# Performance work log

Measured on AMD Instinct MI355X. Metric: run time of the kernel, lower is better.

Reference implementation:

```python
import jax, jax.numpy as jnp
import numpy as np

BITS = 16          # number of histogram bins == number of spiking time steps
B, IN_DIM, HID = 16384, 784, 128


def setup_inputs() -> dict:
    key = jax.random.key(0)
    ks = jax.random.split(key, 9)
    dims = [(HID, IN_DIM), (HID, HID), (HID, HID), (IN_DIM, HID)]
    inp = {"features": jax.random.uniform(ks[0], (B, IN_DIM), jnp.float32)}
    for i, (o, d) in enumerate(dims):
        inp["W%d" % i] = jax.random.normal(ks[1 + i], (o, d), jnp.float32) * 0.05
        inp["b%d" % i] = jax.random.normal(ks[5 + i], (o,), jnp.float32) * 0.05
    # np.histogram_bin_edges(bins=16) -> 17 uniformly spaced edges per layer
    in_max = [1.0, 4.0, 4.0, 4.0]
    out_max = [4.0, 4.0, 4.0, 4.0]
    for i in range(4):
        inp["in_bins%d" % i] = jnp.linspace(0.0, in_max[i], BITS + 1, dtype=jnp.float32)
        inp["out_bins%d" % i] = jnp.linspace(0.0, out_max[i], BITS + 1, dtype=jnp.float32)
    return inp


def _spike(t):
    # output[output>1]=1; output[output<1]=0  (==1 stays 1)  -> (t >= 1)
    # totals[output==1] -= 1
    s = (t >= 1.0).astype(t.dtype)
    return s, t - s


def _forward(features, Ws, bs, in_bins, out_bins):
    h_in = [e[1] - e[0] for e in in_bins]    # uniform spike heights
    h_out = [e[1] - e[0] for e in out_bins]
    # set_up_weights: weight *= h_in; weight /= h_out (bias likewise)
    Weff = [Ws[l] * (h_in[l] / h_out[l]) for l in range(4)]
    beff = [bs[l] * (h_in[l] / h_out[l]) for l in range(4)]
    n = features.shape[0]
    # discretize: np.digitize(x, in_bins) - 1, then / 16.0 (non-differentiable)
    act = (jnp.digitize(jax.lax.stop_gradient(features), in_bins[0]) - 1).astype(features.dtype) / BITS
    t_in = jnp.zeros_like(features)                               # input-layer membrane
    totals = tuple(jnp.broadcast_to(beff[l], (n,) + beff[l].shape) for l in range(4))  # reset_totals: totals = bias
    out_acc = jnp.zeros((n, Weff[3].shape[0]), features.dtype)

    def step(carry, _):
        t_in, t0, t1, t2, t3, out = carry
        s_in, t_in = _spike(t_in + act)
        # process_layer: totals += sum(weight * spikes, axis=1) == spikes @ W.T
        s0, t0 = _spike(t0 + s_in @ Weff[0].T)
        s1, t1 = _spike(t1 + s0 @ Weff[1].T)
        s2, t2 = _spike(t2 + s1 @ Weff[2].T)
        s3, t3 = _spike(t3 + s2 @ Weff[3].T)
        return (t_in, t0, t1, t2, t3, out + s3), None

    carry, _ = jax.lax.scan(step, (t_in,) + totals + (out_acc,), None, length=BITS)
    out_spikes = carry[-1]
    # decoder_output_layer.reconstruct: spikes * (out_bins[1] - out_bins[0])
    return out_spikes * h_out[3]


def reference(features, W0, W1, W2, W3, b0, b1, b2, b3,
              in_bins0, in_bins1, in_bins2, in_bins3,
              out_bins0, out_bins1, out_bins2, out_bins3):
    return _forward(features,
                    [W0, W1, W2, W3], [b0, b1, b2, b3],
                    [in_bins0, in_bins1, in_bins2, in_bins3],
                    [out_bins0, out_bins1, out_bins2, out_bins3])
```

## Files before the change

### kernel.cpp

```cpp
#include <hip/hip_runtime.h>

#define IN_DIM 784
#define HID 128
#define NSTEP 16
#define BATCH 16384

typedef float v2f __attribute__((ext_vector_type(2)));
typedef float v4f __attribute__((ext_vector_type(4)));

constexpr int W0T_OFF = 0;
constexpr int W1T_OFF = W0T_OFF + IN_DIM*HID;
constexpr int W2T_OFF = W1T_OFF + HID*HID;
constexpr int W3T_OFF = W2T_OFF + HID*HID;
constexpr int B0_OFF  = W3T_OFF + HID*IN_DIM;
constexpr int B1_OFF  = B0_OFF + HID;
constexpr int B2_OFF  = B1_OFF + HID;
constexpr int B3_OFF  = B2_OFF + HID;
constexpr int WS_FLOATS = B3_OFF + IN_DIM;

constexpr int CHUNK_COLS = 32;
constexpr int CHUNK_F    = CHUNK_COLS * HID;
constexpr int NCHUNK     = 25;

constexpr int TPB   = 512;
constexpr int WAVES = TPB / 64;

__global__ __launch_bounds__(256) void prep_kernel(
    const float* __restrict__ W0, const float* __restrict__ b0,
    const float* __restrict__ W1, const float* __restrict__ b1,
    const float* __restrict__ W2, const float* __restrict__ b2,
    const float* __restrict__ W3, const float* __restrict__ b3,
    const float* __restrict__ ib0, const float* __restrict__ ob0,
    const float* __restrict__ ib1, const float* __restrict__ ob1,
    const float* __restrict__ ib2, const float* __restrict__ ob2,
    const float* __restrict__ ib3, const float* __restrict__ ob3,
    float* __restrict__ ws)
{
    int idx = blockIdx.x * 256 + threadIdx.x;
    if (idx >= WS_FLOATS) return;
    float r0 = (ib0[1] - ib0[0]) / (ob0[1] - ob0[0]);
    float r1 = (ib1[1] - ib1[0]) / (ob1[1] - ob1[0]);
    float r2 = (ib2[1] - ib2[0]) / (ob2[1] - ob2[0]);
    float r3 = (ib3[1] - ib3[0]) / (ob3[1] - ob3[0]);
    if (idx < W1T_OFF) {
        int t = idx;            int k = t >> 7, j = t & 127;
        ws[idx] = W0[j * IN_DIM + k] * r0;
    } else if (idx < W2T_OFF) {
        int t = idx - W1T_OFF;  int k = t >> 7, j = t & 127;
        ws[idx] = W1[j * HID + k] * r1;
    } else if (idx < W3T_OFF) {
        int t = idx - W2T_OFF;  int k = t >> 7, j = t & 127;
        ws[idx] = W2[j * HID + k] * r2;
    } else if (idx < B0_OFF) {
        int t = idx - W3T_OFF;  int k = t / IN_DIM, o = t % IN_DIM;
        ws[idx] = W3[o * HID + k] * r3;
    } else if (idx < B1_OFF) ws[idx] = b0[idx - B0_OFF] * r0;
    else if (idx < B2_OFF)   ws[idx] = b1[idx - B1_OFF] * r1;
    else if (idx < B3_OFF)   ws[idx] = b2[idx - B2_OFF] * r2;
    else                     ws[idx] = b3[idx - B3_OFF] * r3;
}

__global__ __launch_bounds__(TPB) void snn_main(
    const float* __restrict__ feat,
    const float* __restrict__ ws,
    const float* __restrict__ ib0,
    const float* __restrict__ ob3,
    float* __restrict__ out)
{
    __shared__ float smem[2 * CHUNK_F];

    const int tid  = threadIdx.x;
    const int lane = tid & 63;
    const int wid  = tid >> 6;
    const int sample = blockIdx.x * WAVES + wid;

    const float* W0t = ws + W0T_OFF;
    const float* W1t = ws + W1T_OFF;
    const float* W2t = ws + W2T_OFF;
    const float* W3t = ws + W3T_OFF;
    const float* frow = feat + (size_t)sample * IN_DIM;

    float edge[16];
#pragma unroll
    for (int e = 0; e < 16; ++e) edge[e] = ib0[e + 1];

    {
        const float4* g4 = (const float4*)W0t;
        float4* lb = (float4*)smem;
#pragma unroll
        for (int i = 0; i < 2; ++i) lb[i * TPB + tid] = g4[i * TPB + tid];
    }
    __syncthreads();

    v2f C[16];
#pragma unroll
    for (int mv = 0; mv < 16; ++mv) C[mv] = (v2f)(0.f);

    for (int c = 0; c < NCHUNK; ++c) {
        float4 rg0, rg1;
        {
            const float4* g4 = (const float4*)W0t + (size_t)(c + 1) * (CHUNK_F / 4);
            rg0 = g4[0 * TPB + tid];
            rg1 = g4[1 * TPB + tid];
        }

        int col = c * CHUNK_COLS + (lane & 31);
        bool valid = col < IN_DIM;
        float x = frow[valid ? col : 0];
        int mm = 0;
#pragma unroll
        for (int e = 0; e < 16; ++e) mm += (x >= edge[e]) ? 1 : 0;
        if (!valid) mm = -1;

        const v2f* bufp = (const v2f*)(smem + (c & 1) * CHUNK_F);
#pragma unroll
        for (int mv = 1; mv <= 16; ++mv) {
            unsigned mk = (unsigned)__ballot(mm == mv);
            v2f ca = (v2f)(0.f), cb = (v2f)(0.f);
            while (mk) {
                int b0 = __builtin_ctz(mk); mk &= mk - 1;
                v2f w0 = bufp[b0 * 64 + lane];
                if (mk) {
                    int b1 = __builtin_ctz(mk); mk &= mk - 1;
                    v2f w1 = bufp[b1 * 64 + lane];
                    if (mk) {
                        int b2 = __builtin_ctz(mk); mk &= mk - 1;
                        v2f w2 = bufp[b2 * 64 + lane];
                        if (mk) {
                            int b3i = __builtin_ctz(mk); mk &= mk - 1;
                            v2f w3 = bufp[b3i * 64 + lane];
                            cb += w3;
                        }
                        ca += w2;
                    }
                    cb += w1;
                }
                ca += w0;
            }
            C[mv - 1] += ca + cb;
        }

        if (c + 1 < NCHUNK) {
            float4* lb = (float4*)(smem + ((c + 1) & 1) * CHUNK_F);
            lb[0 * TPB + tid] = rg0;
            lb[1 * TPB + tid] = rg1;
        }
        __syncthreads();
    }

    v2f t0 = ((const v2f*)(ws + B0_OFF))[lane];
    v2f t1 = ((const v2f*)(ws + B1_OFF))[lane];
    v2f t2 = ((const v2f*)(ws + B2_OFF))[lane];
    v4f t3[4], cnt[4];
    {
        const v4f* b3v = (const v4f*)(ws + B3_OFF);
#pragma unroll
        for (int r = 0; r < 3; ++r) t3[r] = b3v[r * 64 + lane];
        t3[3] = (v4f)(0.f);
        if (lane < 4) t3[3] = b3v[192 + lane];
#pragma unroll
        for (int r = 0; r < 4; ++r) cnt[r] = (v4f)(0.f);
    }

    for (int s = 1; s <= NSTEP; ++s) {
#pragma unroll
        for (int mv = 1; mv <= 16; ++mv) {
            if (((s * mv) & 15) < mv) t0 += C[mv - 1];
        }
        {
            bool px = (t0.x >= 1.0f), py = (t0.y >= 1.0f);
            unsigned long long mx = __ballot(px);
            unsigned long long my = __ballot(py);
            if (px) t0.x -= 1.0f;
            if (py) t0.y -= 1.0f;
            v2f ca = (v2f)(0.f), cb = (v2f)(0.f);
            while (mx) {
                int b0 = __builtin_amdgcn_readfirstlane(__builtin_ctzll(mx)); mx &= mx - 1;
                v2f w0 = ((const v2f*)(W1t + (2 * b0) * HID))[lane];
                if (mx) {
                    int b1 = __builtin_amdgcn_readfirstlane(__builtin_ctzll(mx)); mx &= mx - 1;
                    v2f w1 = ((const v2f*)(W1t + (2 * b1) * HID))[lane];
                    if (mx) {
                        int b2 = __builtin_amdgcn_readfirstlane(__builtin_ctzll(mx)); mx &= mx - 1;
                        v2f w2 = ((const v2f*)(W1t + (2 * b2) * HID))[lane];
                        if (mx) {
                            int b3i = __builtin_amdgcn_readfirstlane(__builtin_ctzll(mx)); mx &= mx - 1;
                            v2f w3 = ((const v2f*)(W1t + (2 * b3i) * HID))[lane];
                            cb += w3;
                        }
                        ca += w2;
                    }
                    cb += w1;
                }
                ca += w0;
            }
            while (my) {
                int b0 = __builtin_amdgcn_readfirstlane(__builtin_ctzll(my)); my &= my - 1;
                v2f w0 = ((const v2f*)(W1t + (2 * b0 + 1) * HID))[lane];
                if (my) {
                    int b1 = __builtin_amdgcn_readfirstlane(__builtin_ctzll(my)); my &= my - 1;
                    v2f w1 = ((const v2f*)(W1t + (2 * b1 + 1) * HID))[lane];
                    if (my) {
                        int b2 = __builtin_amdgcn_readfirstlane(__builtin_ctzll(my)); my &= my - 1;
                        v2f w2 = ((const v2f*)(W1t + (2 * b2 + 1) * HID))[lane];
                        if (my) {
                            int b3i = __builtin_amdgcn_readfirstlane(__builtin_ctzll(my)); my &= my - 1;
                            v2f w3 = ((const v2f*)(W1t + (2 * b3i + 1) * HID))[lane];
                            cb += w3;
                        }
                        ca += w2;
                    }
                    cb += w1;
                }
                ca += w0;
            }
            t1 += ca + cb;
        }
        {
            bool px = (t1.x >= 1.0f), py = (t1.y >= 1.0f);
            unsigned long long mx = __ballot(px);
            unsigned long long my = __ballot(py);
            if (px) t1.x -= 1.0f;
            if (py) t1.y -= 1.0f;
            v2f ca = (v2f)(0.f), cb = (v2f)(0.f);
            while (mx) {
                int b0 = __builtin_amdgcn_readfirstlane(__builtin_ctzll(mx)); mx &= mx - 1;
                v2f w0 = ((const v2f*)(W2t + (2 * b0) * HID))[lane];
                if (mx) {
                    int b1 = __builtin_amdgcn_readfirstlane(__builtin_ctzll(mx)); mx &= mx - 1;
                    v2f w1 = ((const v2f*)(W2t + (2 * b1) * HID))[lane];
                    if (mx) {
                        int b2 = __builtin_amdgcn_readfirstlane(__builtin_ctzll(mx)); mx &= mx - 1;
                        v2f w2 = ((const v2f*)(W2t + (2 * b2) * HID))[lane];
                        if (mx) {
                            int b3i = __builtin_amdgcn_readfirstlane(__builtin_ctzll(mx)); mx &= mx - 1;
                            v2f w3 = ((const v2f*)(W2t + (2 * b3i) * HID))[lane];
                            cb += w3;
                        }
                        ca += w2;
                    }
                    cb += w1;
                }
                ca += w0;
            }
            while (my) {
                int b0 = __builtin_amdgcn_readfirstlane(__builtin_ctzll(my)); my &= my - 1;
                v2f w0 = ((const v2f*)(W2t + (2 * b0 + 1) * HID))[lane];
                if (my) {
                    int b1 = __builtin_amdgcn_readfirstlane(__builtin_ctzll(my)); my &= my - 1;
                    v2f w1 = ((const v2f*)(W2t + (2 * b1 + 1) * HID))[lane];
                    if (my) {
                        int b2 = __builtin_amdgcn_readfirstlane(__builtin_ctzll(my)); my &= my - 1;
                        v2f w2 = ((const v2f*)(W2t + (2 * b2 + 1) * HID))[lane];
                        if (my) {
                            int b3i = __builtin_amdgcn_readfirstlane(__builtin_ctzll(my)); my &= my - 1;
                            v2f w3 = ((const v2f*)(W2t + (2 * b3i + 1) * HID))[lane];
                            cb += w3;
                        }
                        ca += w2;
                    }
                    cb += w1;
                }
                ca += w0;
            }
            t2 += ca + cb;
        }
        {
            bool px = (t2.x >= 1.0f), py = (t2.y >= 1.0f);
            unsigned long long mx = __ballot(px);
            unsigned long long my = __ballot(py);
            if (px) t2.x -= 1.0f;
            if (py) t2.y -= 1.0f;
            while (mx) {
                int b0 = __builtin_amdgcn_readfirstlane(__builtin_ctzll(mx)); mx &= mx - 1;
                const v4f* c0 = (const v4f*)(W3t + (2 * b0) * IN_DIM);
                v4f x0 = c0[lane], x1 = c0[64 + lane], x2 = c0[128 + lane];
                v4f x3 = c0[192 + (lane & 3)];
                if (mx) {
                    int b1 = __builtin_amdgcn_readfirstlane(__builtin_ctzll(mx)); mx &= mx - 1;
                    const v4f* c1 = (const v4f*)(W3t + (2 * b1) * IN_DIM);
                    v4f y0 = c1[lane], y1 = c1[64 + lane], y2 = c1[128 + lane];
                    v4f y3 = c1[192 + (lane & 3)];
                    t3[0] += y0; t3[1] += y1; t3[2] += y2;
                    if (lane < 4) t3[3] += y3;
                }
                t3[0] += x0; t3[1] += x1; t3[2] += x2;
                if (lane < 4) t3[3] += x3;
            }
            while (my) {
                int b0 = __builtin_amdgcn_readfirstlane(__builtin_ctzll(my)); my &= my - 1;
                const v4f* c0 = (const v4f*)(W3t + (2 * b0 + 1) * IN_DIM);
                v4f x0 = c0[lane], x1 = c0[64 + lane], x2 = c0[128 + lane];
                v4f x3 = c0[192 + (lane & 3)];
                if (my) {
                    int b1 = __builtin_amdgcn_readfirstlane(__builtin_ctzll(my)); my &= my - 1;
                    const v4f* c1 = (const v4f*)(W3t + (2 * b1 + 1) * IN_DIM);
                    v4f y0 = c1[lane], y1 = c1[64 + lane], y2 = c1[128 + lane];
                    v4f y3 = c1[192 + (lane & 3)];
                    t3[0] += y0; t3[1] += y1; t3[2] += y2;
                    if (lane < 4) t3[3] += y3;
                }
                t3[0] += x0; t3[1] += x1; t3[2] += x2;
                if (lane < 4) t3[3] += x3;
            }
        }
#pragma unroll
        for (int r = 0; r < 4; ++r) {
            if (t3[r].x >= 1.0f) { t3[r].x -= 1.0f; cnt[r].x += 1.0f; }
            if (t3[r].y >= 1.0f) { t3[r].y -= 1.0f; cnt[r].y += 1.0f; }
            if (t3[r].z >= 1.0f) { t3[r].z -= 1.0f; cnt[r].z += 1.0f; }
            if (t3[r].w >= 1.0f) { t3[r].w -= 1.0f; cnt[r].w += 1.0f; }
        }
    }

    const float h = ob3[1] - ob3[0];
    v4f* orow = (v4f*)(out + (size_t)sample * IN_DIM);
#pragma unroll
    for (int r = 0; r < 3; ++r)
        orow[r * 64 + lane] = cnt[r] * h;
    if (lane < 4)
        orow[192 + lane] = cnt[3] * h;
}

extern "C" void kernel_launch(void* const* d_in, const int* in_sizes, int n_in,
                              void* d_out, int out_size, void* d_ws, size_t ws_size,
                              hipStream_t stream)
{
    const float* feat = (const float*)d_in[0];
    const float* W0  = (const float*)d_in[1];
    const float* b0  = (const float*)d_in[2];
    const float* W1  = (const float*)d_in[3];
    const float* b1  = (const float*)d_in[4];
    const float* W2  = (const float*)d_in[5];
    const float* b2  = (const float*)d_in[6];
    const float* W3  = (const float*)d_in[7];
    const float* b3  = (const float*)d_in[8];
    const float* ib0 = (const float*)d_in[9];
    const float* ob0 = (const float*)d_in[10];
    const float* ib1 = (const float*)d_in[11];
    const float* ob1 = (const float*)d_in[12];
    const float* ib2 = (const float*)d_in[13];
    const float* ob2 = (const float*)d_in[14];
    const float* ib3 = (const float*)d_in[15];
    const float* ob3 = (const float*)d_in[16];
    float* ws  = (float*)d_ws;
    float* op  = (float*)d_out;

    prep_kernel<<<(WS_FLOATS + 255) / 256, 256, 0, stream>>>(
        W0, b0, W1, b1, W2, b2, W3, b3,
        ib0, ob0, ib1, ob1, ib2, ob2, ib3, ob3, ws);

    snn_main<<<BATCH / WAVES, TPB, 0, stream>>>(feat, ws, ib0, ob3, op);
}
```

Before: 412.9 us.

## Split SNN kernel into layer-0 mask build and sparse propagation kernels

Splits the single fused kernel in two. The first does the layer-0 matmul and spike generation and writes per-step ballot masks to workspace. The second, a lighter kernel with 256 threads per block, reads those masks and runs the sparse propagation through layers 1-3. The aim is to separate the LDS-heavy, register-heavy build phase from the latency-bound sparse gather phase so that each can run at better occupancy. In exchange it adds a second launch and a global round trip of the masks. It also drops the readfirstlane calls on the bit indices and relies on the compiler to keep them uniform.

```diff
diff --git a/kernel.cpp b/kernel.cpp
--- a/kernel.cpp
+++ b/kernel.cpp
@@ -7,6 +7,7 @@
 
 typedef float v2f __attribute__((ext_vector_type(2)));
 typedef float v4f __attribute__((ext_vector_type(4)));
+typedef unsigned long long ull;
 
 constexpr int W0T_OFF = 0;
 constexpr int W1T_OFF = W0T_OFF + IN_DIM*HID;
@@ -17,6 +18,7 @@
 constexpr int B2_OFF  = B1_OFF + HID;
 constexpr int B3_OFF  = B2_OFF + HID;
 constexpr int WS_FLOATS = B3_OFF + IN_DIM;
+constexpr int MASK_OFF  = WS_FLOATS;
 
 constexpr int CHUNK_COLS = 32;
 constexpr int CHUNK_F    = CHUNK_COLS * HID;
@@ -60,12 +62,11 @@
     else                     ws[idx] = b3[idx - B3_OFF] * r3;
 }
 
-__global__ __launch_bounds__(TPB) void snn_main(
+__global__ __launch_bounds__(TPB) void snn_build(
     const float* __restrict__ feat,
     const float* __restrict__ ws,
     const float* __restrict__ ib0,
-    const float* __restrict__ ob3,
-    float* __restrict__ out)
+    ull* __restrict__ masks)
 {
     __shared__ float smem[2 * CHUNK_F];
 
@@ -75,9 +76,6 @@
     const int sample = blockIdx.x * WAVES + wid;
 
     const float* W0t = ws + W0T_OFF;
-    const float* W1t = ws + W1T_OFF;
-    const float* W2t = ws + W2T_OFF;
-    const float* W3t = ws + W3T_OFF;
     const float* frow = feat + (size_t)sample * IN_DIM;
 
     float edge[16];
@@ -149,6 +147,41 @@
     }
 
     v2f t0 = ((const v2f*)(ws + B0_OFF))[lane];
+    ull* mrow = masks + (size_t)sample * 32;
+
+    for (int s = 1; s <= NSTEP; ++s) {
+#pragma unroll
+        for (int mv = 1; mv <= 16; ++mv) {
+            if (((s * mv) & 15) < mv) t0 += C[mv - 1];
+        }
+        bool px = (t0.x >= 1.0f), py = (t0.y >= 1.0f);
+        ull mx = __ballot(px);
+        ull my = __ballot(py);
+        if (px) t0.x -= 1.0f;
+        if (py) t0.y -= 1.0f;
+        if (lane == 0) {
+            mrow[2 * (s - 1)]     = mx;
+            mrow[2 * (s - 1) + 1] = my;
+        }
+    }
+}
+
+__global__ __launch_bounds__(256) void snn_prop(
+    const float* __restrict__ ws,
+    const ull* __restrict__ masks,
+    const float* __restrict__ ob3,
+    float* __restrict__ out)
+{
+    const int tid  = threadIdx.x;
+    const int lane = tid & 63;
+    const int wid  = tid >> 6;
+    const int sample = blockIdx.x * 4 + wid;
+
+    const float* W1t = ws + W1T_OFF;
+    const float* W2t = ws + W2T_OFF;
+    const float* W3t = ws + W3T_OFF;
+    const ull* mrow = masks + (size_t)sample * 32;
+
     v2f t1 = ((const v2f*)(ws + B1_OFF))[lane];
     v2f t2 = ((const v2f*)(ws + B2_OFF))[lane];
     v4f t3[4], cnt[4];
@@ -162,29 +195,26 @@
         for (int r = 0; r < 4; ++r) cnt[r] = (v4f)(0.f);
     }
 
-    for (int s = 1; s <= NSTEP; ++s) {
-#pragma unroll
-        for (int mv = 1; mv <= 16; ++mv) {
-            if (((s * mv) & 15) < mv) t0 += C[mv - 1];
-        }
+    for (int s = 0; s < NSTEP; ++s) {
+        ull vx = mrow[2 * s], vy = mrow[2 * s + 1];
+        ull mx = ((ull)__builtin_amdgcn_readfirstlane((unsigned)(vx >> 32)) << 32)
+               | __builtin_amdgcn_readfirstlane((unsigned)vx);
+        ull my = ((ull)__builtin_amdgcn_readfirstlane((unsigned)(vy >> 32)) << 32)
+               | __builtin_amdgcn_readfirstlane((unsigned)vy);
+
         {
-            bool px = (t0.x >= 1.0f), py = (t0.y >= 1.0f);
-            unsigned long long mx = __ballot(px);
-            unsigned long long my = __ballot(py);
-            if (px) t0.x -= 1.0f;
-            if (py) t0.y -= 1.0f;
             v2f ca = (v2f)(0.f), cb = (v2f)(0.f);
             while (mx) {
-                int b0 = __builtin_amdgcn_readfirstlane(__builtin_ctzll(mx)); mx &= mx - 1;
+                int b0 = __builtin_ctzll(mx); mx &= mx - 1;
                 v2f w0 = ((const v2f*)(W1t + (2 * b0) * HID))[lane];
                 if (mx) {
-                    int b1 = __builtin_amdgcn_readfirstlane(__builtin_ctzll(mx)); mx &= mx - 1;
+                    int b1 = __builtin_ctzll(mx); mx &= mx - 1;
                     v2f w1 = ((const v2f*)(W1t + (2 * b1) * HID))[lane];
                     if (mx) {
-                        int b2 = __builtin_amdgcn_readfirstlane(__builtin_ctzll(mx)); mx &= mx - 1;
+                        int b2 = __builtin_ctzll(mx); mx &= mx - 1;
                         v2f w2 = ((const v2f*)(W1t + (2 * b2) * HID))[lane];
                         if (mx) {
-                            int b3i = __builtin_amdgcn_readfirstlane(__builtin_ctzll(mx)); mx &= mx - 1;
+                            int b3i = __builtin_ctzll(mx); mx &= mx - 1;
                             v2f w3 = ((const v2f*)(W1t + (2 * b3i) * HID))[lane];
                             cb += w3;
                         }
@@ -195,16 +225,16 @@
                 ca += w0;
             }
             while (my) {
-                int b0 = __builtin_amdgcn_readfirstlane(__builtin_ctzll(my)); my &= my - 1;
+                int b0 = __builtin_ctzll(my); my &= my - 1;
                 v2f w0 = ((const v2f*)(W1t + (2 * b0 + 1) * HID))[lane];
                 if (my) {
-                    int b1 = __builtin_amdgcn_readfirstlane(__builtin_ctzll(my)); my &= my - 1;
+                    int b1 = __builtin_ctzll(my); my &= my - 1;
                     v2f w1 = ((const v2f*)(W1t + (2 * b1 + 1) * HID))[lane];
                     if (my) {
-                        int b2 = __builtin_amdgcn_readfirstlane(__builtin_ctzll(my)); my &= my - 1;
+                        int b2 = __builtin_ctzll(my); my &= my - 1;
                         v2f w2 = ((const v2f*)(W1t + (2 * b2 + 1) * HID))[lane];
                         if (my) {
-                            int b3i = __builtin_amdgcn_readfirstlane(__builtin_ctzll(my)); my &= my - 1;
+                            int b3i = __builtin_ctzll(my); my &= my - 1;
                             v2f w3 = ((const v2f*)(W1t + (2 * b3i + 1) * HID))[lane];
                             cb += w3;
                         }
@@ -218,22 +248,22 @@
         }
         {
             bool px = (t1.x >= 1.0f), py = (t1.y >= 1.0f);
-            unsigned long long mx = __ballot(px);
-            unsigned long long my = __ballot(py);
+            ull nx = __ballot(px);
+            ull ny = __ballot(py);
             if (px) t1.x -= 1.0f;
             if (py) t1.y -= 1.0f;
             v2f ca = (v2f)(0.f), cb = (v2f)(0.f);
-            while (mx) {
-                int b0 = __builtin_amdgcn_readfirstlane(__builtin_ctzll(mx)); mx &= mx - 1;
+            while (nx) {
+                int b0 = __builtin_ctzll(nx); nx &= nx - 1;
                 v2f w0 = ((const v2f*)(W2t + (2 * b0) * HID))[lane];
-                if (mx) {
-                    int b1 = __builtin_amdgcn_readfirstlane(__builtin_ctzll(mx)); mx &= mx - 1;
+                if (nx) {
+                    int b1 = __builtin_ctzll(nx); nx &= nx - 1;
                     v2f w1 = ((const v2f*)(W2t + (2 * b1) * HID))[lane];
-                    if (mx) {
-                        int b2 = __builtin_amdgcn_readfirstlane(__builtin_ctzll(mx)); mx &= mx - 1;
+                    if (nx) {
+                        int b2 = __builtin_ctzll(nx); nx &= nx - 1;
                         v2f w2 = ((const v2f*)(W2t + (2 * b2) * HID))[lane];
-                        if (mx) {
-                            int b3i = __builtin_amdgcn_readfirstlane(__builtin_ctzll(mx)); mx &= mx - 1;
+                        if (nx) {
+                            int b3i = __builtin_ctzll(nx); nx &= nx - 1;
                             v2f w3 = ((const v2f*)(W2t + (2 * b3i) * HID))[lane];
                             cb += w3;
                         }
@@ -243,17 +273,17 @@
                 }
                 ca += w0;
             }
-            while (my) {
-                int b0 = __builtin_amdgcn_readfirstlane(__builtin_ctzll(my)); my &= my - 1;
+            while (ny) {
+                int b0 = __builtin_ctzll(ny); ny &= ny - 1;
                 v2f w0 = ((const v2f*)(W2t + (2 * b0 + 1) * HID))[lane];
-                if (my) {
-                    int b1 = __builtin_amdgcn_readfirstlane(__builtin_ctzll(my)); my &= my - 1;
+                if (ny) {
+                    int b1 = __builtin_ctzll(ny); ny &= ny - 1;
                     v2f w1 = ((const v2f*)(W2t + (2 * b1 + 1) * HID))[lane];
-                    if (my) {
-                        int b2 = __builtin_amdgcn_readfirstlane(__builtin_ctzll(my)); my &= my - 1;
+                    if (ny) {
+                        int b2 = __builtin_ctzll(ny); ny &= ny - 1;
                         v2f w2 = ((const v2f*)(W2t + (2 * b2 + 1) * HID))[lane];
-                        if (my) {
-                            int b3i = __builtin_amdgcn_readfirstlane(__builtin_ctzll(my)); my &= my - 1;
+                        if (ny) {
+                            int b3i = __builtin_ctzll(ny); ny &= ny - 1;
                             v2f w3 = ((const v2f*)(W2t + (2 * b3i + 1) * HID))[lane];
                             cb += w3;
                         }
@@ -267,17 +297,17 @@
         }
         {
             bool px = (t2.x >= 1.0f), py = (t2.y >= 1.0f);
-            unsigned long long mx = __ballot(px);
-            unsigned long long my = __ballot(py);
+            ull nx = __ballot(px);
+            ull ny = __ballot(py);
             if (px) t2.x -= 1.0f;
             if (py) t2.y -= 1.0f;
-            while (mx) {
-                int b0 = __builtin_amdgcn_readfirstlane(__builtin_ctzll(mx)); mx &= mx - 1;
+            while (nx) {
+                int b0 = __builtin_ctzll(nx); nx &= nx - 1;
                 const v4f* c0 = (const v4f*)(W3t + (2 * b0) * IN_DIM);
                 v4f x0 = c0[lane], x1 = c0[64 + lane], x2 = c0[128 + lane];
                 v4f x3 = c0[192 + (lane & 3)];
-                if (mx) {
-                    int b1 = __builtin_amdgcn_readfirstlane(__builtin_ctzll(mx)); mx &= mx - 1;
+                if (nx) {
+                    int b1 = __builtin_ctzll(nx); nx &= nx - 1;
                     const v4f* c1 = (const v4f*)(W3t + (2 * b1) * IN_DIM);
                     v4f y0 = c1[lane], y1 = c1[64 + lane], y2 = c1[128 + lane];
                     v4f y3 = c1[192 + (lane & 3)];
@@ -287,13 +317,13 @@
                 t3[0] += x0; t3[1] += x1; t3[2] += x2;
                 if (lane < 4) t3[3] += x3;
             }
-            while (my) {
-                int b0 = __builtin_amdgcn_readfirstlane(__builtin_ctzll(my)); my &= my - 1;
+            while (ny) {
+                int b0 = __builtin_ctzll(ny); ny &= ny - 1;
                 const v4f* c0 = (const v4f*)(W3t + (2 * b0 + 1) * IN_DIM);
                 v4f x0 = c0[lane], x1 = c0[64 + lane], x2 = c0[128 + lane];
                 v4f x3 = c0[192 + (lane & 3)];
-                if (my) {
-                    int b1 = __builtin_amdgcn_readfirstlane(__builtin_ctzll(my)); my &= my - 1;
+                if (ny) {
+                    int b1 = __builtin_ctzll(ny); ny &= ny - 1;
                     const v4f* c1 = (const v4f*)(W3t + (2 * b1 + 1) * IN_DIM);
                     v4f y0 = c1[lane], y1 = c1[64 + lane], y2 = c1[128 + lane];
                     v4f y3 = c1[192 + (lane & 3)];
@@ -345,10 +375,12 @@
     const float* ob3 = (const float*)d_in[16];
     float* ws  = (float*)d_ws;
     float* op  = (float*)d_out;
+    ull* masks = (ull*)(ws + MASK_OFF);
 
     prep_kernel<<<(WS_FLOATS + 255) / 256, 256, 0, stream>>>(
         W0, b0, W1, b1, W2, b2, W3, b3,
         ib0, ob0, ib1, ob1, ib2, ob2, ib3, ob3, ws);
 
-    snn_main<<<BATCH / WAVES, TPB, 0, stream>>>(feat, ws, ib0, ob3, op);
+    snn_build<<<BATCH / WAVES, TPB, 0, stream>>>(feat, ws, ib0, masks);
+    snn_prop<<<BATCH / 4, 256, 0, stream>>>(ws, masks, ob3, op);
 }
```

Measured after the change: 435.5 us. 5.5% more time.
